# Kernel tuning notes

Measured on AMD Instinct MI355X. Metric: run time of the kernel, lower is better.

## Reference

```python
import jax, jax.numpy as jnp
import numpy as np

B = 8192
D = 4096  # input_size == hidden_size (required by the module's forward)
H = 4096


def setup_inputs() -> dict:
    key = jax.random.key(0)
    ks = jax.random.split(key, 14)
    s = 0.02
    inp = {
        "input": jax.random.normal(ks[0], (B, D), dtype=jnp.float32),
        "hidden_state": jax.random.normal(ks[1], (B, H), dtype=jnp.float32),
        # torch nn.Linear weights: [out_features, in_features]
        "w_ir": jax.random.normal(ks[2], (H, D), dtype=jnp.float32) * s,
        "b_ir": jax.random.normal(ks[3], (H,), dtype=jnp.float32) * s,
        "w_iz": jax.random.normal(ks[4], (H, D), dtype=jnp.float32) * s,
        "b_iz": jax.random.normal(ks[5], (H,), dtype=jnp.float32) * s,
        "w_in": jax.random.normal(ks[6], (H, D), dtype=jnp.float32) * s,
        "b_in": jax.random.normal(ks[7], (H,), dtype=jnp.float32) * s,
        "w_hr": jax.random.normal(ks[8], (H, H), dtype=jnp.float32) * s,
        "b_hr": jax.random.normal(ks[9], (H,), dtype=jnp.float32) * s,
        "w_hz": jax.random.normal(ks[10], (H, H), dtype=jnp.float32) * s,
        "b_hz": jax.random.normal(ks[11], (H,), dtype=jnp.float32) * s,
        "w_hn": jax.random.normal(ks[12], (H, H), dtype=jnp.float32) * s,
        "b_hn": jax.random.normal(ks[13], (H,), dtype=jnp.float32) * s,
    }
    return inp


def reference(input, hidden_state, w_ir, b_ir, w_iz, b_iz, w_in, b_in,
              w_hr, b_hr, w_hz, b_hz, w_hn, b_hn):
    # NOTE: faithful to the source: ALL six gates are applied to `input`
    # (the hidden_* gates are also fed `input`, not hidden_state), and the
    # "new" gate uses sigmoid (not tanh).
    # Fuse the six small GEMMs into one batched GEMM: stack weights [6H, D].
    W = jnp.concatenate([w_ir, w_iz, w_in, w_hr, w_hz, w_hn], axis=0)  # [6H, D]
    bvec = jnp.concatenate([b_ir, b_iz, b_in, b_hr, b_hz, b_hn], axis=0)  # [6H]
    g = jnp.einsum('bd,od->bo', input, W) + bvec  # [B, 6H]
    ir, iz, inn, hr, hz, hn = jnp.split(g, 6, axis=-1)
    r = jax.nn.sigmoid(ir + hr)
    z = jax.nn.sigmoid(iz + hz)
    n = jax.nn.sigmoid(inn + r * hn)
    return (1.0 - z) * hidden_state + z * n
```

## Files before the change

kernel.cpp:

```cpp
#include <hip/hip_runtime.h>
#include <hip/hip_bf16.h>


#define THREADS 512
#define B_DIM 8192
#define D_DIM 4096
#define H_DIM 4096
#define BM 256
#define GBN 64
#define BK 64
#define NT (D_DIM / BK)
#define DBUF 65536

#define WS_WR 0
#define WS_WZ 33554432
#define WS_WN 67108864
#define WS_WH 100663296
#define WS_A  134217728
#define WS_NEED 201326592ULL

typedef __attribute__((ext_vector_type(8))) short bf16x8;
typedef __attribute__((ext_vector_type(4))) float f32x4;
typedef __attribute__((ext_vector_type(4))) int i32x4;

__device__ __forceinline__ unsigned f2bf(float f) {
    union { float f; unsigned u; } v; v.f = f;
    return (v.u + 0x7FFFu + ((v.u >> 16) & 1u)) >> 16;
}
__device__ __forceinline__ unsigned pk(float a, float b) {
    return (f2bf(a) & 0xFFFFu) | (f2bf(b) << 16);
}
__device__ __forceinline__ i32x4 pack8(float4 x, float4 y) {
    i32x4 r;
    r[0] = (int)pk(x.x, x.y); r[1] = (int)pk(x.z, x.w);
    r[2] = (int)pk(y.x, y.y); r[3] = (int)pk(y.z, y.w);
    return r;
}
__device__ __forceinline__ float sigmoidf_(float x) {
    return 1.0f / (1.0f + __expf(-x));
}
__device__ __forceinline__ void gld16(const void* g, void* l) {
    __builtin_amdgcn_global_load_lds(
        (const __attribute__((address_space(1))) unsigned*)g,
        (__attribute__((address_space(3))) unsigned*)l, 16, 0, 0);
}

__global__ __launch_bounds__(256) void prep_w_t(
    const float* __restrict__ ir, const float* __restrict__ hr,
    const float* __restrict__ iz, const float* __restrict__ hz,
    const float* __restrict__ inw, const float* __restrict__ hn,
    char* __restrict__ wsbase)
{
    const int tx = threadIdx.x;
    const int R = tx & 15;
    const int c8loc = tx >> 4;
    const int bx = blockIdx.x;
    const int c8blk = bx & 31;
    const int hgrp = bx >> 5;
    const int gy = blockIdx.y;
    const int h  = hgrp * 16 + R;
    const int c8 = c8blk * 16 + c8loc;

    const float* s1 = (gy == 0) ? ir : (gy == 1) ? iz : (gy == 2) ? inw : hn;
    const size_t fi = ((size_t)h * 512 + c8) * 2;
    const float4* p1 = (const float4*)s1;
    float4 a0 = p1[fi], a1 = p1[fi + 1];
    if (gy < 2) {
        const float4* p2 = (const float4*)((gy == 0) ? hr : hz);
        a0 = a0 + p2[fi];
        a1 = a1 + p2[fi + 1];
    }
    const i32x4 v = pack8(a0, a1);
    const int hblk = h >> 6, nfr = (h >> 4) & 3;
    const int t = c8 >> 3, K = (c8 >> 2) & 1, C = c8 & 3;
    const size_t addr = (size_t)gy * 33554432 + (size_t)hblk * 524288
                      + (size_t)t * 8192 + nfr * 2048 + K * 1024 + C * 256 + R * 16;
    *(i32x4*)(wsbase + addr) = v;
}

__global__ __launch_bounds__(256) void prep_a_t(const float* __restrict__ in,
                                                char* __restrict__ abase)
{
    const int tx = threadIdx.x;
    const int R = tx & 15;
    const int c8loc = tx >> 4;
    const int bx = blockIdx.x;
    const int c8blk = bx & 31;
    const int bgrp = bx >> 5;
    const int b  = bgrp * 16 + R;
    const int c8 = c8blk * 16 + c8loc;

    const size_t fi = ((size_t)b * 512 + c8) * 2;
    const float4* p = (const float4*)in;
    const i32x4 v = pack8(p[fi], p[fi + 1]);
    const int bblk = b >> 8, mfr = (b >> 4) & 15;
    const int t = c8 >> 3, K = (c8 >> 2) & 1, C = c8 & 3;
    const size_t addr = (size_t)bblk * 2097152 + (size_t)t * 32768
                      + mfr * 2048 + K * 1024 + C * 256 + R * 16;
    *(i32x4*)(abase + addr) = v;
}

__global__ __launch_bounds__(THREADS, 2) void gru_bf16(
    const char* __restrict__ Abf, const char* __restrict__ Wr,
    const char* __restrict__ Wz, const char* __restrict__ Wn,
    const char* __restrict__ Wh,
    const float* __restrict__ hidden,
    const float* __restrict__ b_ir, const float* __restrict__ b_iz,
    const float* __restrict__ b_in, const float* __restrict__ b_hr,
    const float* __restrict__ b_hz, const float* __restrict__ b_hn,
    float* __restrict__ out)
{
    __shared__ __attribute__((aligned(128))) char smem[2 * DBUF];

    const int tid  = threadIdx.x;
    const int lane = tid & 63;
    const int wid  = tid >> 6;
    const int wm   = wid >> 2;
    const int wn   = wid & 3;

    const int nb   = (int)blockIdx.x;
    const int bblk = nb & 31;
    const int hblk = nb >> 5;
    const int b0 = bblk * BM;
    const int h0 = hblk * GBN;

    const int sg  = wid >> 1;
    const int sn0 = (wid & 1) * 2;
    const char* gWsel = (sg == 0) ? Wr : (sg == 1) ? Wz : (sg == 2) ? Wn : Wh;
    const char* pA = Abf + (size_t)bblk * 2097152 + (size_t)(2 * wid) * 2048 + (lane << 4);
    const char* pB = gWsel + (size_t)hblk * 524288 + (size_t)sn0 * 2048 + (lane << 4);
    const int dA = (2 * wid) * 2048;
    const int dB = 32768 + sg * 8192 + sn0 * 2048;

    f32x4 acc[4][8];
#pragma unroll
    for (int g = 0; g < 4; ++g)
#pragma unroll
        for (int m = 0; m < 8; ++m) acc[g][m] = (f32x4)0.0f;

#define STAGE_A(t, d) do { const size_t ko = (size_t)(t) * 32768;              \
        gld16(pA + ko,        smem + (d) + dA);                                \
        gld16(pA + ko + 1024, smem + (d) + dA + 1024);                         \
        gld16(pA + ko + 2048, smem + (d) + dA + 2048);                         \
        gld16(pA + ko + 3072, smem + (d) + dA + 3072);                         \
    } while (0)

#define STAGE_B(t, d) do { const size_t ko = (size_t)(t) * 8192;               \
        gld16(pB + ko,        smem + (d) + dB);                                \
        gld16(pB + ko + 1024, smem + (d) + dB + 1024);                         \
        gld16(pB + ko + 2048, smem + (d) + dB + 2048);                         \
        gld16(pB + ko + 3072, smem + (d) + dB + 3072);                         \
    } while (0)

#define RD_AF(dst, mhq) do {                                                   \
        _Pragma("unroll")                                                      \
        for (int mf = 0; mf < 4; ++mf)                                         \
            _Pragma("unroll")                                                  \
            for (int kk = 0; kk < 2; ++kk)                                     \
                dst[mf][kk] = *(const bf16x8*)(cb + ((wm * 8 + (mhq) * 4 + mf) * 2 + kk) * 1024 + (lane << 4)); \
    } while (0)

#define RD_FB(g) do {                                                          \
        _Pragma("unroll")                                                      \
        for (int kk = 0; kk < 2; ++kk)                                         \
            fb[g][kk] = *(const bf16x8*)(cb + 32768 + (g) * 8192 + (wn * 2 + kk) * 1024 + (lane << 4)); \
    } while (0)

#define MM(acc_, a_, b_) acc_ = __builtin_amdgcn_mfma_f32_16x16x32_bf16(a_, b_, acc_, 0, 0, 0)

#define MFMA_CL(src, g0_, ab_) do {                                            \
        __builtin_amdgcn_s_setprio(1);                                         \
        _Pragma("unroll")                                                      \
        for (int g = (g0_); g < (g0_) + 2; ++g)                                \
            _Pragma("unroll")                                                  \
            for (int mf = 0; mf < 4; ++mf)                                     \
                _Pragma("unroll")                                              \
                for (int kk = 0; kk < 2; ++kk)                                 \
                    MM(acc[g][(ab_) * 4 + mf], src[mf][kk], fb[g][kk]);        \
        __builtin_amdgcn_s_setprio(0);                                         \
    } while (0)

#define SB0 __builtin_amdgcn_sched_barrier(0)

    STAGE_A(0, 0);
    STAGE_B(0, 0);
    asm volatile("s_waitcnt vmcnt(0)" ::: "memory");
    __builtin_amdgcn_s_barrier();

#pragma unroll 1
    for (int t = 0; t < NT; ++t) {
        const int p = t & 1;
        const char* cb = smem + p * DBUF;
        const int d = (p ^ 1) * DBUF;
        const bool stg = (t < NT - 1);
        bf16x8 afA[4][2], afB[4][2], fb[4][2];

        RD_AF(afA, 0);
        RD_FB(0); RD_FB(1);
        if (stg) STAGE_A(t + 1, d);
        SB0;
        RD_FB(2); RD_FB(3);
        if (stg) STAGE_B(t + 1, d);
        asm volatile("s_waitcnt lgkmcnt(4)" ::: "memory");
        SB0;
        MFMA_CL(afA, 0, 0);
        asm volatile("s_waitcnt lgkmcnt(0)" ::: "memory");
        SB0;
        RD_AF(afB, 1);
        MFMA_CL(afA, 2, 0);
        asm volatile("s_waitcnt lgkmcnt(0)" ::: "memory");
        SB0;
        MFMA_CL(afB, 0, 1);
        MFMA_CL(afB, 2, 1);
        if (stg) { asm volatile("s_waitcnt vmcnt(0)" ::: "memory"); }
        SB0;
        __builtin_amdgcn_s_barrier();
    }

    const int r4 = (lane >> 4) * 4;
    const int cn = lane & 15;
    {
        const int h = h0 + wn * 16 + cn;
        const float br = b_ir[h] + b_hr[h];
        const float bz = b_iz[h] + b_hz[h];
        const float bn = b_in[h];
        const float bh = b_hn[h];
#pragma unroll
        for (int m = 0; m < 8; ++m) {
            const int brow = b0 + wm * 128 + m * 16 + r4;
#pragma unroll
            for (int j = 0; j < 4; ++j) {
                const size_t idx = (size_t)(brow + j) * H_DIM + h;
                const float r = sigmoidf_(acc[0][m][j] + br);
                const float z = sigmoidf_(acc[1][m][j] + bz);
                const float n = sigmoidf_(acc[2][m][j] + bn + r * (acc[3][m][j] + bh));
                out[idx] = (1.0f - z) * hidden[idx] + z * n;
            }
        }
    }
#undef STAGE_A
#undef STAGE_B
#undef RD_AF
#undef RD_FB
#undef MM
#undef MFMA_CL
#undef SB0
}

__global__ __launch_bounds__(THREADS, 2) void gru_fused_f32(
    const float* __restrict__ input, const float* __restrict__ hidden,
    const float* __restrict__ w_ir, const float* __restrict__ b_ir,
    const float* __restrict__ w_iz, const float* __restrict__ b_iz,
    const float* __restrict__ w_in, const float* __restrict__ b_in,
    const float* __restrict__ w_hr, const float* __restrict__ b_hr,
    const float* __restrict__ w_hz, const float* __restrict__ b_hz,
    const float* __restrict__ w_hn, const float* __restrict__ b_hn,
    float* __restrict__ out)
{
    __shared__ int smem[2 * 10240];
    const int tid  = threadIdx.x;
    const int lane = tid & 63;
    const int wid  = tid >> 6;
    const int wm   = wid >> 2;
    const int wn   = wid & 3;
    const int bblk = blockIdx.x & 63;
    const int hblk = blockIdx.x >> 6;
    const int b0 = bblk * 128;
    const int h0 = hblk * 128;
    const int srow = tid >> 2;
    const int sc   = tid & 3;
    const float4* gA  = (const float4*)(input + (size_t)(b0 + srow) * D_DIM + sc * 8);
    const size_t woff = (size_t)(h0 + srow) * D_DIM + sc * 8;
    const float4* gIr = (const float4*)(w_ir + woff);
    const float4* gHr = (const float4*)(w_hr + woff);
    const float4* gIz = (const float4*)(w_iz + woff);
    const float4* gHz = (const float4*)(w_hz + woff);
    const float4* gIn = (const float4*)(w_in + woff);
    const float4* gHn = (const float4*)(w_hn + woff);
    const int wr_ints = (srow >> 4) * 256 + ((sc * 16 + (srow & 15)) * 4);

    f32x4 accR[4][2], accZ[4][2], accN[4][2], accH[4][2];
#pragma unroll
    for (int mf = 0; mf < 4; ++mf)
#pragma unroll
        for (int nf = 0; nf < 2; ++nf) {
            accR[mf][nf] = (f32x4)0.0f; accZ[mf][nf] = (f32x4)0.0f;
            accN[mf][nf] = (f32x4)0.0f; accH[mf][nf] = (f32x4)0.0f;
        }
    float4 La0, La1, Lr0, Lr1, Lr2, Lr3, Lz0, Lz1, Lz2, Lz3, Ln0, Ln1, Lh0, Lh1;
#define LOADREGS(s) do { const int o = (s) * 8;                          \
        La0 = gA[o];  La1 = gA[o + 1];                                   \
        Lr0 = gIr[o]; Lr1 = gIr[o + 1]; Lr2 = gHr[o]; Lr3 = gHr[o + 1];  \
        Lz0 = gIz[o]; Lz1 = gIz[o + 1]; Lz2 = gHz[o]; Lz3 = gHz[o + 1];  \
        Ln0 = gIn[o]; Ln1 = gIn[o + 1];                                  \
        Lh0 = gHn[o]; Lh1 = gHn[o + 1]; } while (0)
#define WRITELDS(pp) do { const int wb = (pp) * 10240 + wr_ints;          \
        *(i32x4*)&smem[wb]        = pack8(La0, La1);                      \
        *(i32x4*)&smem[wb + 2048] = pack8(Lr0 + Lr2, Lr1 + Lr3);          \
        *(i32x4*)&smem[wb + 4096] = pack8(Lz0 + Lz2, Lz1 + Lz3);          \
        *(i32x4*)&smem[wb + 6144] = pack8(Ln0, Ln1);                      \
        *(i32x4*)&smem[wb + 8192] = pack8(Lh0, Lh1); } while (0)
#define COMPUTE(pp) do {                                                  \
        const int cb = (pp) * 10240;                                      \
        const bf16x8* Af = (const bf16x8*)&smem[cb];                      \
        const bf16x8* Br = (const bf16x8*)&smem[cb + 2048];               \
        const bf16x8* Bz = (const bf16x8*)&smem[cb + 4096];               \
        const bf16x8* Bn = (const bf16x8*)&smem[cb + 6144];               \
        const bf16x8* Bh = (const bf16x8*)&smem[cb + 8192];               \
        bf16x8 afr[4];                                                    \
        _Pragma("unroll")                                                 \
        for (int mf = 0; mf < 4; ++mf)                                    \
            afr[mf] = Af[(wm * 4 + mf) * 64 + lane];                      \
        _Pragma("unroll")                                                 \
        for (int nf = 0; nf < 2; ++nf) {                                  \
            const int bi = (wn * 2 + nf) * 64 + lane;                     \
            bf16x8 fr = Br[bi], fz = Bz[bi], fn = Bn[bi], fh = Bh[bi];    \
            _Pragma("unroll")                                             \
            for (int mf = 0; mf < 4; ++mf) {                              \
                accR[mf][nf] = __builtin_amdgcn_mfma_f32_16x16x32_bf16(afr[mf], fr, accR[mf][nf], 0, 0, 0); \
                accZ[mf][nf] = __builtin_amdgcn_mfma_f32_16x16x32_bf16(afr[mf], fz, accZ[mf][nf], 0, 0, 0); \
                accN[mf][nf] = __builtin_amdgcn_mfma_f32_16x16x32_bf16(afr[mf], fn, accN[mf][nf], 0, 0, 0); \
                accH[mf][nf] = __builtin_amdgcn_mfma_f32_16x16x32_bf16(afr[mf], fh, accH[mf][nf], 0, 0, 0); \
            }                                                             \
        } } while (0)
    LOADREGS(0);
    WRITELDS(0);
    __syncthreads();
#pragma unroll 1
    for (int s = 0; s < 128; ++s) {
        if (s + 1 < 128) LOADREGS(s + 1);
        COMPUTE(s & 1);
        if (s + 1 < 128) { WRITELDS((s + 1) & 1); __syncthreads(); }
    }
    const int r4 = (lane >> 4) * 4;
    const int cn = lane & 15;
#pragma unroll
    for (int nf = 0; nf < 2; ++nf) {
        const int h = h0 + wn * 32 + nf * 16 + cn;
        const float br = b_ir[h] + b_hr[h];
        const float bz = b_iz[h] + b_hz[h];
        const float bn = b_in[h];
        const float bh = b_hn[h];
#pragma unroll
        for (int mf = 0; mf < 4; ++mf) {
            const int brow = b0 + wm * 64 + mf * 16 + r4;
#pragma unroll
            for (int j = 0; j < 4; ++j) {
                const size_t idx = (size_t)(brow + j) * H_DIM + h;
                const float r = sigmoidf_(accR[mf][nf][j] + br);
                const float z = sigmoidf_(accZ[mf][nf][j] + bz);
                const float n = sigmoidf_(accN[mf][nf][j] + bn + r * (accH[mf][nf][j] + bh));
                out[idx] = (1.0f - z) * hidden[idx] + z * n;
            }
        }
    }
#undef LOADREGS
#undef WRITELDS
#undef COMPUTE
}

extern "C" void kernel_launch(void* const* d_in, const int* in_sizes, int n_in,
                              void* d_out, int out_size, void* d_ws, size_t ws_size,
                              hipStream_t stream) {
    const float* input  = (const float*)d_in[0];
    const float* hidden = (const float*)d_in[1];
    const float* w_ir = (const float*)d_in[2];  const float* b_ir = (const float*)d_in[3];
    const float* w_iz = (const float*)d_in[4];  const float* b_iz = (const float*)d_in[5];
    const float* w_in = (const float*)d_in[6];  const float* b_in = (const float*)d_in[7];
    const float* w_hr = (const float*)d_in[8];  const float* b_hr = (const float*)d_in[9];
    const float* w_hz = (const float*)d_in[10]; const float* b_hz = (const float*)d_in[11];
    const float* w_hn = (const float*)d_in[12]; const float* b_hn = (const float*)d_in[13];
    float* out = (float*)d_out;

    if (ws_size >= WS_NEED) {
        char* ws = (char*)d_ws;
        prep_w_t<<<dim3(8192, 4), dim3(256), 0, stream>>>(
            w_ir, w_hr, w_iz, w_hz, w_in, w_hn, ws);
        prep_a_t<<<dim3(16384), dim3(256), 0, stream>>>(input, ws + WS_A);
        gru_bf16<<<dim3((B_DIM / BM) * (H_DIM / GBN)), dim3(THREADS), 0, stream>>>(
            ws + WS_A, ws + WS_WR, ws + WS_WZ, ws + WS_WN, ws + WS_WH,
            hidden, b_ir, b_iz, b_in, b_hr, b_hz, b_hn, out);
    } else {
        gru_fused_f32<<<dim3(2048), dim3(THREADS), 0, stream>>>(
            input, hidden, w_ir, b_ir, w_iz, b_iz, w_in, b_in,
            w_hr, b_hr, w_hz, b_hz, w_hn, b_hn, out);
    }
}
```

Before: 998.7 us.

## Switch GRU GEMM to 32x32x16 bf16 MFMA with matching fragment layouts

Replaces the 16x16x32 MFMA tiling with 32x32x16 MFMA instructions. Each wave now computes a 64x64 tile (two 32-row fragments by the 4 gates times 32 columns) instead of 128x16. The prep kernels rewrite the pre-packed A and W workspace layouts to match the 32-lane fragment ordering, and the epilogue row/column mapping is updated. The larger MFMA is meant to cut LDS fragment reads per FLOP and the instruction count, at the cost of a different register and bank-access pattern.

```diff
diff --git a/kernel.cpp b/kernel.cpp
--- a/kernel.cpp
+++ b/kernel.cpp
@@ -21,6 +21,7 @@
 
 typedef __attribute__((ext_vector_type(8))) short bf16x8;
 typedef __attribute__((ext_vector_type(4))) float f32x4;
+typedef __attribute__((ext_vector_type(16))) float f32x16;
 typedef __attribute__((ext_vector_type(4))) int i32x4;
 
 __device__ __forceinline__ unsigned f2bf(float f) {
@@ -52,14 +53,14 @@
     char* __restrict__ wsbase)
 {
     const int tx = threadIdx.x;
-    const int R = tx & 15;
-    const int c8loc = tx >> 4;
+    const int C32 = tx & 31;
+    const int c8loc = tx >> 5;
     const int bx = blockIdx.x;
-    const int c8blk = bx & 31;
-    const int hgrp = bx >> 5;
+    const int c8blk = bx & 63;
+    const int hgrp = bx >> 6;
     const int gy = blockIdx.y;
-    const int h  = hgrp * 16 + R;
-    const int c8 = c8blk * 16 + c8loc;
+    const int h  = hgrp * 32 + C32;
+    const int c8 = c8blk * 8 + c8loc;
 
     const float* s1 = (gy == 0) ? ir : (gy == 1) ? iz : (gy == 2) ? inw : hn;
     const size_t fi = ((size_t)h * 512 + c8) * 2;
@@ -71,10 +72,10 @@
         a1 = a1 + p2[fi + 1];
     }
     const i32x4 v = pack8(a0, a1);
-    const int hblk = h >> 6, nfr = (h >> 4) & 3;
-    const int t = c8 >> 3, K = (c8 >> 2) & 1, C = c8 & 3;
-    const size_t addr = (size_t)gy * 33554432 + (size_t)hblk * 524288
-                      + (size_t)t * 8192 + nfr * 2048 + K * 1024 + C * 256 + R * 16;
+    const int t = c8 >> 3, kf = (c8 >> 1) & 3, kg = c8 & 1;
+    const size_t addr = (size_t)gy * 33554432 + (size_t)(h >> 6) * 524288
+                      + (size_t)t * 8192 + (((h >> 5) & 1) * 4 + kf) * 1024
+                      + (kg * 32 + (h & 31)) * 16;
     *(i32x4*)(wsbase + addr) = v;
 }
 
@@ -82,21 +83,21 @@
                                                 char* __restrict__ abase)
 {
     const int tx = threadIdx.x;
-    const int R = tx & 15;
-    const int c8loc = tx >> 4;
+    const int R32 = tx & 31;
+    const int c8loc = tx >> 5;
     const int bx = blockIdx.x;
-    const int c8blk = bx & 31;
-    const int bgrp = bx >> 5;
-    const int b  = bgrp * 16 + R;
-    const int c8 = c8blk * 16 + c8loc;
+    const int c8blk = bx & 63;
+    const int bgrp = bx >> 6;
+    const int b  = bgrp * 32 + R32;
+    const int c8 = c8blk * 8 + c8loc;
 
     const size_t fi = ((size_t)b * 512 + c8) * 2;
     const float4* p = (const float4*)in;
     const i32x4 v = pack8(p[fi], p[fi + 1]);
-    const int bblk = b >> 8, mfr = (b >> 4) & 15;
-    const int t = c8 >> 3, K = (c8 >> 2) & 1, C = c8 & 3;
-    const size_t addr = (size_t)bblk * 2097152 + (size_t)t * 32768
-                      + mfr * 2048 + K * 1024 + C * 256 + R * 16;
+    const int t = c8 >> 3, kf = (c8 >> 1) & 3, kg = c8 & 1;
+    const size_t addr = (size_t)(b >> 8) * 2097152 + (size_t)t * 32768
+                      + (((b >> 5) & 7) * 4 + kf) * 1024
+                      + (kg * 32 + (b & 31)) * 16;
     *(i32x4*)(abase + addr) = v;
 }
 
@@ -115,8 +116,8 @@
     const int tid  = threadIdx.x;
     const int lane = tid & 63;
     const int wid  = tid >> 6;
-    const int wm   = wid >> 2;
-    const int wn   = wid & 3;
+    const int wm   = wid >> 1;
+    const int wq   = wid & 1;
 
     const int nb   = (int)blockIdx.x;
     const int bblk = nb & 31;
@@ -124,59 +125,57 @@
     const int b0 = bblk * BM;
     const int h0 = hblk * GBN;
 
-    const int sg  = wid >> 1;
-    const int sn0 = (wid & 1) * 2;
-    const char* gWsel = (sg == 0) ? Wr : (sg == 1) ? Wz : (sg == 2) ? Wn : Wh;
-    const char* pA = Abf + (size_t)bblk * 2097152 + (size_t)(2 * wid) * 2048 + (lane << 4);
-    const char* pB = gWsel + (size_t)hblk * 524288 + (size_t)sn0 * 2048 + (lane << 4);
-    const int dA = (2 * wid) * 2048;
-    const int dB = 32768 + sg * 8192 + sn0 * 2048;
-
-    f32x4 acc[4][8];
+    const int sg = wid >> 1;
+    const int hb = wid & 1;
+    const char* gW = (sg == 0) ? Wr : (sg == 1) ? Wz : (sg == 2) ? Wn : Wh;
+    const char* pA = Abf + (size_t)bblk * 2097152 + (size_t)wid * 4096 + (lane << 4);
+    const char* pB = gW + (size_t)hblk * 524288 + (size_t)hb * 4096 + (lane << 4);
+    const int dA = wid * 4096;
+    const int dB = 32768 + sg * 8192 + hb * 4096;
+
+    f32x16 acc[4][2];
 #pragma unroll
     for (int g = 0; g < 4; ++g)
 #pragma unroll
-        for (int m = 0; m < 8; ++m) acc[g][m] = (f32x4)0.0f;
-
-#define STAGE_A(t, d) do { const size_t ko = (size_t)(t) * 32768;              \
-        gld16(pA + ko,        smem + (d) + dA);                                \
-        gld16(pA + ko + 1024, smem + (d) + dA + 1024);                         \
-        gld16(pA + ko + 2048, smem + (d) + dA + 2048);                         \
-        gld16(pA + ko + 3072, smem + (d) + dA + 3072);                         \
-    } while (0)
-
-#define STAGE_B(t, d) do { const size_t ko = (size_t)(t) * 8192;               \
-        gld16(pB + ko,        smem + (d) + dB);                                \
-        gld16(pB + ko + 1024, smem + (d) + dB + 1024);                         \
-        gld16(pB + ko + 2048, smem + (d) + dB + 2048);                         \
-        gld16(pB + ko + 3072, smem + (d) + dB + 3072);                         \
-    } while (0)
-
-#define RD_AF(dst, mhq) do {                                                   \
+        for (int m = 0; m < 2; ++m) acc[g][m] = (f32x16)0.0f;
+
+#define STAGE_A(t, d) do { const char* s_ = pA + (size_t)(t) * 32768;          \
+        gld16(s_,        smem + (d) + dA);                                     \
+        gld16(s_ + 1024, smem + (d) + dA + 1024);                              \
+        gld16(s_ + 2048, smem + (d) + dA + 2048);                              \
+        gld16(s_ + 3072, smem + (d) + dA + 3072);                              \
+    } while (0)
+
+#define STAGE_B(t, d) do { const char* s_ = pB + (size_t)(t) * 8192;           \
+        gld16(s_,        smem + (d) + dB);                                     \
+        gld16(s_ + 1024, smem + (d) + dB + 1024);                              \
+        gld16(s_ + 2048, smem + (d) + dB + 2048);                              \
+        gld16(s_ + 3072, smem + (d) + dB + 3072);                              \
+    } while (0)
+
+#define RD_AF do {                                                             \
         _Pragma("unroll")                                                      \
-        for (int mf = 0; mf < 4; ++mf)                                         \
+        for (int m = 0; m < 2; ++m)                                            \
             _Pragma("unroll")                                                  \
-            for (int kk = 0; kk < 2; ++kk)                                     \
-                dst[mf][kk] = *(const bf16x8*)(cb + ((wm * 8 + (mhq) * 4 + mf) * 2 + kk) * 1024 + (lane << 4)); \
-    } while (0)
-
-#define RD_FB(g) do {                                                          \
+            for (int kf = 0; kf < 4; ++kf)                                     \
+                af[m][kf] = *(const bf16x8*)(cb + ((2 * wm + m) * 4 + kf) * 1024 + (lane << 4)); \
+    } while (0)
+
+#define RD_FB(dst, gi, g) do {                                                 \
         _Pragma("unroll")                                                      \
-        for (int kk = 0; kk < 2; ++kk)                                         \
-            fb[g][kk] = *(const bf16x8*)(cb + 32768 + (g) * 8192 + (wn * 2 + kk) * 1024 + (lane << 4)); \
-    } while (0)
-
-#define MM(acc_, a_, b_) acc_ = __builtin_amdgcn_mfma_f32_16x16x32_bf16(a_, b_, acc_, 0, 0, 0)
-
-#define MFMA_CL(src, g0_, ab_) do {                                            \
+        for (int kf = 0; kf < 4; ++kf)                                         \
+            dst[gi][kf] = *(const bf16x8*)(cb + 32768 + (g) * 8192 + (wq * 4 + kf) * 1024 + (lane << 4)); \
+    } while (0)
+
+#define MM(acc_, a_, b_) acc_ = __builtin_amdgcn_mfma_f32_32x32x16_bf16(a_, b_, acc_, 0, 0, 0)
+
+#define MFMA_CL(src, gi, g) do {                                               \
         __builtin_amdgcn_s_setprio(1);                                         \
         _Pragma("unroll")                                                      \
-        for (int g = (g0_); g < (g0_) + 2; ++g)                                \
+        for (int m = 0; m < 2; ++m)                                            \
             _Pragma("unroll")                                                  \
-            for (int mf = 0; mf < 4; ++mf)                                     \
-                _Pragma("unroll")                                              \
-                for (int kk = 0; kk < 2; ++kk)                                 \
-                    MM(acc[g][(ab_) * 4 + mf], src[mf][kk], fb[g][kk]);        \
+            for (int kf = 0; kf < 4; ++kf)                                     \
+                MM(acc[g][m], af[m][kf], src[gi][kf]);                         \
         __builtin_amdgcn_s_setprio(0);                                         \
     } while (0)
 
@@ -193,44 +192,45 @@
         const char* cb = smem + p * DBUF;
         const int d = (p ^ 1) * DBUF;
         const bool stg = (t < NT - 1);
-        bf16x8 afA[4][2], afB[4][2], fb[4][2];
-
-        RD_AF(afA, 0);
-        RD_FB(0); RD_FB(1);
+        bf16x8 af[2][4], fbA[2][4], fbB[2][4];
+
+        RD_AF;
+        RD_FB(fbA, 0, 0);
         if (stg) STAGE_A(t + 1, d);
         SB0;
-        RD_FB(2); RD_FB(3);
+        RD_FB(fbA, 1, 1);
         if (stg) STAGE_B(t + 1, d);
         asm volatile("s_waitcnt lgkmcnt(4)" ::: "memory");
         SB0;
-        MFMA_CL(afA, 0, 0);
+        MFMA_CL(fbA, 0, 0);
         asm volatile("s_waitcnt lgkmcnt(0)" ::: "memory");
         SB0;
-        RD_AF(afB, 1);
-        MFMA_CL(afA, 2, 0);
+        RD_FB(fbB, 0, 2);
+        RD_FB(fbB, 1, 3);
+        MFMA_CL(fbA, 1, 1);
         asm volatile("s_waitcnt lgkmcnt(0)" ::: "memory");
         SB0;
-        MFMA_CL(afB, 0, 1);
-        MFMA_CL(afB, 2, 1);
+        MFMA_CL(fbB, 0, 2);
+        MFMA_CL(fbB, 1, 3);
         if (stg) { asm volatile("s_waitcnt vmcnt(0)" ::: "memory"); }
         SB0;
         __builtin_amdgcn_s_barrier();
     }
 
-    const int r4 = (lane >> 4) * 4;
-    const int cn = lane & 15;
+    const int col = lane & 31;
+    const int rb  = 4 * (lane >> 5);
     {
-        const int h = h0 + wn * 16 + cn;
+        const int h = h0 + wq * 32 + col;
         const float br = b_ir[h] + b_hr[h];
         const float bz = b_iz[h] + b_hz[h];
         const float bn = b_in[h];
         const float bh = b_hn[h];
 #pragma unroll
-        for (int m = 0; m < 8; ++m) {
-            const int brow = b0 + wm * 128 + m * 16 + r4;
-#pragma unroll
-            for (int j = 0; j < 4; ++j) {
-                const size_t idx = (size_t)(brow + j) * H_DIM + h;
+        for (int m = 0; m < 2; ++m) {
+#pragma unroll
+            for (int j = 0; j < 16; ++j) {
+                const int row = b0 + wm * 64 + m * 32 + (j & 3) + 8 * (j >> 2) + rb;
+                const size_t idx = (size_t)row * H_DIM + h;
                 const float r = sigmoidf_(acc[0][m][j] + br);
                 const float z = sigmoidf_(acc[1][m][j] + bz);
                 const float n = sigmoidf_(acc[2][m][j] + bn + r * (acc[3][m][j] + bh));
@@ -247,7 +247,7 @@
 #undef SB0
 }
 
-__global__ __launch_bounds__(THREADS, 2) void gru_fused_f32(
+__global__ __launch_bounds__(512, 2) void gru_fused_f32(
     const float* __restrict__ input, const float* __restrict__ hidden,
     const float* __restrict__ w_ir, const float* __restrict__ b_ir,
     const float* __restrict__ w_iz, const float* __restrict__ b_iz,
@@ -381,7 +381,7 @@
             ws + WS_A, ws + WS_WR, ws + WS_WZ, ws + WS_WN, ws + WS_WH,
             hidden, b_ir, b_iz, b_in, b_hr, b_hz, b_hn, out);
     } else {
-        gru_fused_f32<<<dim3(2048), dim3(THREADS), 0, stream>>>(
+        gru_fused_f32<<<dim3(2048), dim3(512), 0, stream>>>(
             input, hidden, w_ir, b_ir, w_iz, b_iz, w_in, b_in,
             w_hr, b_hr, w_hz, b_hz, w_hn, b_hn, out);
     }
```

After: 1.180 ms. 1.18x slower.
